# Performance work log

Measured on AMD Instinct MI355X. Metric: run time of the kernel, lower is better.

## Reference

```python
import jax, jax.numpy as jnp
from jax import lax
import numpy as np

BATCH, DIM, HID, NSTEPS = 32768, 128, 256, 50

def setup_inputs() -> dict:
    key = jax.random.key(0)
    k1, k2, k3 = jax.random.split(key, 3)
    inputs = jax.random.normal(k1, (BATCH, DIM), dtype=jnp.float32)
    # increasing timestamps over [0, 1] -> 50 Euler steps of dt = 0.02
    timestamps = jnp.linspace(0.0, 1.0, NSTEPS + 1, dtype=jnp.float32)
    # small init keeps the Euler trajectory stable
    W1 = jax.random.normal(k2, (DIM, HID), dtype=jnp.float32) * 0.05
    b1 = jnp.zeros((HID,), dtype=jnp.float32)
    W2 = jax.random.normal(k3, (HID, DIM), dtype=jnp.float32) * 0.05
    b2 = jnp.zeros((DIM,), dtype=jnp.float32)
    return {"inputs": inputs, "timestamps": timestamps, "W1": W1, "b1": b1, "W2": W2, "b2": b2}

def reference(inputs, timestamps, W1, b1, W2, b2):
    """Euler integration of dh/dt = f(h) = tanh(h@W1+b1)@W2+b2; returns final state h(T).
    Matches AdjointODEFunc.forward (which returns states[-1])."""
    dts = timestamps[1:] - timestamps[:-1]  # [NSTEPS]

    def f(h):  # vector field (time-invariant MLP)
        return jnp.tanh(h @ W1 + b1) @ W2 + b2

    def step(h, dt):
        return h + dt * f(h), None

    h_final, _ = lax.scan(step, inputs, dts)
    return h_final
```

## Files before the change

### kernel.cpp

```cpp
#include <hip/hip_runtime.h>


typedef __attribute__((ext_vector_type(8))) short short8;
typedef __attribute__((ext_vector_type(4))) float float4v;
typedef __attribute__((ext_vector_type(4))) int int4v;

union FB { int4v i; short8 s; };

#define W1F_OFF 0
#define W2F_OFF 65536
#define B1_OFF  131072
#define DT_OFF  132096
#define LDS_BYTES 132352

#define TSCALE 2.8853900817779268f

__device__ __forceinline__ unsigned rne2(float x) {
  unsigned u = __float_as_uint(x);
  return u + 0x7fffu + ((u >> 16) & 1u);
}

#if __has_builtin(__builtin_amdgcn_cvt_pk_bf16_f32)
__device__ __forceinline__ int pk2(float lo, float hi) {
  return __builtin_bit_cast(int, __builtin_amdgcn_cvt_pk_bf16_f32(lo, hi));
}
#else
__device__ __forceinline__ int pk2(float lo, float hi) {
  return (int)__builtin_amdgcn_perm(rne2(hi), rne2(lo), 0x07060302u);
}
#endif

__device__ __forceinline__ int4v packfrag(float4v e, float4v o) {
  int4v f;
  f.x = pk2(e.x, e.y);
  f.y = pk2(e.z, e.w);
  f.z = pk2(o.x, o.y);
  f.w = pk2(o.z, o.w);
  return f;
}

#define MFMA16(a, b, c) __builtin_amdgcn_mfma_f32_16x16x32_bf16(a, b, c, 0, 0, 0)

extern "C" __global__ __launch_bounds__(512)
void ode_kernel(const float* __restrict__ inp, const float* __restrict__ ts,
                const float* __restrict__ W1, const float* __restrict__ b1,
                const float* __restrict__ W2, const float* __restrict__ b2,
                float* __restrict__ out) {
  __shared__ __align__(16) char ldsb[LDS_BYTES];
  float* b1f = (float*)(ldsb + B1_OFF);
  float* dtf = (float*)(ldsb + DT_OFF);

  const int tid = threadIdx.x;
  const int lane = tid & 63, wave = tid >> 6;
  const int ln = lane & 15;
  const int q = lane >> 4;
  const int row = blockIdx.x * 128 + wave * 16 + ln;

  #pragma unroll 1
  for (int it = 0; it < 8; it++) {
    const int pi = it * 512 + tid;
    const int fid = pi >> 6, L = pi & 63;
    const int nt = fid >> 2, c = fid & 3;
    const int lf = L & 15, qf = L >> 4;
    const int n = nt * 16 + lf;
    const int kb = c * 32 + qf * 4;
    float v0 = W1[(kb + 0) * 256 + n] * TSCALE;
    float v1 = W1[(kb + 1) * 256 + n] * TSCALE;
    float v2 = W1[(kb + 2) * 256 + n] * TSCALE;
    float v3 = W1[(kb + 3) * 256 + n] * TSCALE;
    float v4 = W1[(kb + 16) * 256 + n] * TSCALE;
    float v5 = W1[(kb + 17) * 256 + n] * TSCALE;
    float v6 = W1[(kb + 18) * 256 + n] * TSCALE;
    float v7 = W1[(kb + 19) * 256 + n] * TSCALE;
    int4v d = {pk2(v0, v1), pk2(v2, v3), pk2(v4, v5), pk2(v6, v7)};
    *(int4v*)(ldsb + W1F_OFF + pi * 16) = d;
  }
  #pragma unroll 1
  for (int it = 0; it < 8; it++) {
    const int pi = it * 512 + tid;
    const int fid = pi >> 6, L = pi & 63;
    const int p = fid >> 3, tb = fid & 7;
    const int lf = L & 15, qf = L >> 4;
    const int d_out = tb * 16 + lf;
    const int kb = p * 32 + qf * 4;
    float v0 = W2[(kb + 0) * 128 + d_out];
    float v1 = W2[(kb + 1) * 128 + d_out];
    float v2 = W2[(kb + 2) * 128 + d_out];
    float v3 = W2[(kb + 3) * 128 + d_out];
    float v4 = W2[(kb + 16) * 128 + d_out];
    float v5 = W2[(kb + 17) * 128 + d_out];
    float v6 = W2[(kb + 18) * 128 + d_out];
    float v7 = W2[(kb + 19) * 128 + d_out];
    int4v d = {pk2(v0, v1), pk2(v2, v3), pk2(v4, v5), pk2(v6, v7)};
    *(int4v*)(ldsb + W2F_OFF + pi * 16) = d;
  }
  if (tid < 256) b1f[tid] = b1[tid] * TSCALE;
  if (tid < 50) dtf[tid] = ts[tid + 1] - ts[tid];

  float4v b2v[8];
  #pragma unroll
  for (int tb = 0; tb < 8; tb++)
    b2v[tb] = *(const float4v*)&b2[tb * 16 + q * 4];

  float4v h4[8];
  #pragma unroll
  for (int tb = 0; tb < 8; tb++)
    h4[tb] = *(const float4v*)&inp[row * 128 + tb * 16 + q * 4];

  __syncthreads();

  const int4v* w1f = (const int4v*)(ldsb + W1F_OFF) + lane;
  const int4v* w2f = (const int4v*)(ldsb + W2F_OFF) + lane;

  #pragma unroll 1
  for (int s = 0; s < 50; s++) {
    const float dt = dtf[s];
    const float m2dt = -2.0f * dt;

    FB hb[4];
    #pragma unroll
    for (int kc = 0; kc < 4; kc++)
      hb[kc].i = packfrag(h4[2 * kc], h4[2 * kc + 1]);

    #pragma unroll 1
    for (int p = 0; p < 8; p++) {
      const int nt0 = 2 * p, nt1 = 2 * p + 1;
      FB wA[4], wB[4];
      #pragma unroll
      for (int c = 0; c < 4; c++) {
        wA[c].i = w1f[(nt0 * 4 + c) * 64];
        wB[c].i = w1f[(nt1 * 4 + c) * 64];
      }
      float4v g0 = *(const float4v*)&b1f[nt0 * 16 + q * 4];
      float4v g1 = *(const float4v*)&b1f[nt1 * 16 + q * 4];
      #pragma unroll
      for (int c = 0; c < 4; c++) {
        g0 = MFMA16(wA[c].s, hb[c].s, g0);
        g1 = MFMA16(wB[c].s, hb[c].s, g1);
      }

      FB w2r[8];
      #pragma unroll
      for (int tb = 0; tb < 8; tb++)
        w2r[tb].i = w2f[(p * 8 + tb) * 64];

      float4v a0, a1;
      #pragma unroll
      for (int r = 0; r < 4; r++) {
        a0[r] = fmaf(__builtin_amdgcn_rcpf(__builtin_amdgcn_exp2f(g0[r]) + 1.0f), m2dt, dt);
        a1[r] = fmaf(__builtin_amdgcn_rcpf(__builtin_amdgcn_exp2f(g1[r]) + 1.0f), m2dt, dt);
      }
      FB af;
      af.i = packfrag(a0, a1);

      #pragma unroll
      for (int tb = 0; tb < 8; tb++)
        h4[tb] = MFMA16(w2r[tb].s, af.s, h4[tb]);
    }

    #pragma unroll
    for (int tb = 0; tb < 8; tb++)
      #pragma unroll
      for (int r = 0; r < 4; r++)
        h4[tb][r] = fmaf(dt, b2v[tb][r], h4[tb][r]);
  }

  #pragma unroll
  for (int tb = 0; tb < 8; tb++)
    *(float4v*)&out[row * 128 + tb * 16 + q * 4] = h4[tb];
}

extern "C" void kernel_launch(void* const* d_in, const int* in_sizes, int n_in,
                              void* d_out, int out_size, void* d_ws, size_t ws_size,
                              hipStream_t stream) {
  const float* inp = (const float*)d_in[0];
  const float* ts  = (const float*)d_in[1];
  const float* W1  = (const float*)d_in[2];
  const float* b1  = (const float*)d_in[3];
  const float* W2  = (const float*)d_in[4];
  const float* b2  = (const float*)d_in[5];
  hipLaunchKernelGGL(ode_kernel, dim3(256), dim3(512), 0, stream,
                     inp, ts, W1, b1, W2, b2, (float*)d_out);
}
```

Before: 316.6 us.

## Switch MLP matmuls from bf16 to fp8 MFMA with scaled weights

Weights, hidden state, and activations are now quantized to fp8 (with a ×16 scale on weights and activations) and use the 16x16x32 fp8 MFMA instead of bf16. This halves LDS footprint and fragment register size. It also moves b1 into registers and accumulates the second matmul into a separate fp32 accumulator before the dt-scaled update. The aim is to cut MFMA and LDS traffic per step, at a significant accuracy risk: fp8 quantization of the state h compounds over 50 Euler steps.

```diff
diff --git a/kernel.cpp b/kernel.cpp
--- a/kernel.cpp
+++ b/kernel.cpp
@@ -1,45 +1,33 @@
 #include <hip/hip_runtime.h>
 
 
-typedef __attribute__((ext_vector_type(8))) short short8;
 typedef __attribute__((ext_vector_type(4))) float float4v;
-typedef __attribute__((ext_vector_type(4))) int int4v;
+typedef __attribute__((ext_vector_type(2))) int int2v;
 
-union FB { int4v i; short8 s; };
+union F8 { long l; int2v i; };
 
 #define W1F_OFF 0
-#define W2F_OFF 65536
-#define B1_OFF  131072
-#define DT_OFF  132096
-#define LDS_BYTES 132352
+#define W2F_OFF 32768
+#define DT_OFF  65536
+#define LDS_BYTES 65792
 
 #define TSCALE 2.8853900817779268f
+#define WSC 16.0f
 
-__device__ __forceinline__ unsigned rne2(float x) {
-  unsigned u = __float_as_uint(x);
-  return u + 0x7fffu + ((u >> 16) & 1u);
+__device__ __forceinline__ int pk4_fp8(float a, float b, float c, float d) {
+  int v = __builtin_amdgcn_cvt_pk_fp8_f32(a, b, 0, false);
+  v = __builtin_amdgcn_cvt_pk_fp8_f32(c, d, v, true);
+  return v;
 }
 
-#if __has_builtin(__builtin_amdgcn_cvt_pk_bf16_f32)
-__device__ __forceinline__ int pk2(float lo, float hi) {
-  return __builtin_bit_cast(int, __builtin_amdgcn_cvt_pk_bf16_f32(lo, hi));
-}
-#else
-__device__ __forceinline__ int pk2(float lo, float hi) {
-  return (int)__builtin_amdgcn_perm(rne2(hi), rne2(lo), 0x07060302u);
-}
-#endif
-
-__device__ __forceinline__ int4v packfrag(float4v e, float4v o) {
-  int4v f;
-  f.x = pk2(e.x, e.y);
-  f.y = pk2(e.z, e.w);
-  f.z = pk2(o.x, o.y);
-  f.w = pk2(o.z, o.w);
-  return f;
+__device__ __forceinline__ long packfrag8(float4v e, float4v o) {
+  F8 f;
+  f.i.x = pk4_fp8(e.x, e.y, e.z, e.w);
+  f.i.y = pk4_fp8(o.x, o.y, o.z, o.w);
+  return f.l;
 }
 
-#define MFMA16(a, b, c) __builtin_amdgcn_mfma_f32_16x16x32_bf16(a, b, c, 0, 0, 0)
+#define MFMA8(a, b, c) __builtin_amdgcn_mfma_f32_16x16x32_fp8_fp8(a, b, c, 0, 0, 0)
 
 extern "C" __global__ __launch_bounds__(512)
 void ode_kernel(const float* __restrict__ inp, const float* __restrict__ ts,
@@ -47,7 +35,6 @@
                 const float* __restrict__ W2, const float* __restrict__ b2,
                 float* __restrict__ out) {
   __shared__ __align__(16) char ldsb[LDS_BYTES];
-  float* b1f = (float*)(ldsb + B1_OFF);
   float* dtf = (float*)(ldsb + DT_OFF);
 
   const int tid = threadIdx.x;
@@ -64,16 +51,12 @@
     const int lf = L & 15, qf = L >> 4;
     const int n = nt * 16 + lf;
     const int kb = c * 32 + qf * 4;
-    float v0 = W1[(kb + 0) * 256 + n] * TSCALE;
-    float v1 = W1[(kb + 1) * 256 + n] * TSCALE;
-    float v2 = W1[(kb + 2) * 256 + n] * TSCALE;
-    float v3 = W1[(kb + 3) * 256 + n] * TSCALE;
-    float v4 = W1[(kb + 16) * 256 + n] * TSCALE;
-    float v5 = W1[(kb + 17) * 256 + n] * TSCALE;
-    float v6 = W1[(kb + 18) * 256 + n] * TSCALE;
-    float v7 = W1[(kb + 19) * 256 + n] * TSCALE;
-    int4v d = {pk2(v0, v1), pk2(v2, v3), pk2(v4, v5), pk2(v6, v7)};
-    *(int4v*)(ldsb + W1F_OFF + pi * 16) = d;
+    const float sc = WSC * TSCALE;
+    float4v e = {W1[(kb + 0) * 256 + n] * sc, W1[(kb + 1) * 256 + n] * sc,
+                 W1[(kb + 2) * 256 + n] * sc, W1[(kb + 3) * 256 + n] * sc};
+    float4v o = {W1[(kb + 16) * 256 + n] * sc, W1[(kb + 17) * 256 + n] * sc,
+                 W1[(kb + 18) * 256 + n] * sc, W1[(kb + 19) * 256 + n] * sc};
+    *(long*)(ldsb + W1F_OFF + pi * 8) = packfrag8(e, o);
   }
   #pragma unroll 1
   for (int it = 0; it < 8; it++) {
@@ -81,23 +64,22 @@
     const int fid = pi >> 6, L = pi & 63;
     const int p = fid >> 3, tb = fid & 7;
     const int lf = L & 15, qf = L >> 4;
-    const int d_out = tb * 16 + lf;
+    const int dd = tb * 16 + lf;
     const int kb = p * 32 + qf * 4;
-    float v0 = W2[(kb + 0) * 128 + d_out];
-    float v1 = W2[(kb + 1) * 128 + d_out];
-    float v2 = W2[(kb + 2) * 128 + d_out];
-    float v3 = W2[(kb + 3) * 128 + d_out];
-    float v4 = W2[(kb + 16) * 128 + d_out];
-    float v5 = W2[(kb + 17) * 128 + d_out];
-    float v6 = W2[(kb + 18) * 128 + d_out];
-    float v7 = W2[(kb + 19) * 128 + d_out];
-    int4v d = {pk2(v0, v1), pk2(v2, v3), pk2(v4, v5), pk2(v6, v7)};
-    *(int4v*)(ldsb + W2F_OFF + pi * 16) = d;
+    float4v e = {W2[(kb + 0) * 128 + dd] * WSC, W2[(kb + 1) * 128 + dd] * WSC,
+                 W2[(kb + 2) * 128 + dd] * WSC, W2[(kb + 3) * 128 + dd] * WSC};
+    float4v o = {W2[(kb + 16) * 128 + dd] * WSC, W2[(kb + 17) * 128 + dd] * WSC,
+                 W2[(kb + 18) * 128 + dd] * WSC, W2[(kb + 19) * 128 + dd] * WSC};
+    *(long*)(ldsb + W2F_OFF + pi * 8) = packfrag8(e, o);
   }
-  if (tid < 256) b1f[tid] = b1[tid] * TSCALE;
   if (tid < 50) dtf[tid] = ts[tid + 1] - ts[tid];
 
-  float4v b2v[8];
+  float4v b1v[16], b2v[8];
+  #pragma unroll
+  for (int nt = 0; nt < 16; nt++) {
+    float4v v = *(const float4v*)&b1[nt * 16 + q * 4];
+    b1v[nt] = v * (WSC * TSCALE);
+  }
   #pragma unroll
   for (int tb = 0; tb < 8; tb++)
     b2v[tb] = *(const float4v*)&b2[tb * 16 + q * 4];
@@ -109,60 +91,64 @@
 
   __syncthreads();
 
-  const int4v* w1f = (const int4v*)(ldsb + W1F_OFF) + lane;
-  const int4v* w2f = (const int4v*)(ldsb + W2F_OFF) + lane;
+  const long* w1f = (const long*)(ldsb + W1F_OFF) + lane;
+  const long* w2f = (const long*)(ldsb + W2F_OFF) + lane;
 
   #pragma unroll 1
   for (int s = 0; s < 50; s++) {
     const float dt = dtf[s];
-    const float m2dt = -2.0f * dt;
+    const float dts = dt * (1.0f / 256.0f);
 
-    FB hb[4];
+    long hb[4];
     #pragma unroll
     for (int kc = 0; kc < 4; kc++)
-      hb[kc].i = packfrag(h4[2 * kc], h4[2 * kc + 1]);
+      hb[kc] = packfrag8(h4[2 * kc], h4[2 * kc + 1]);
+
+    float4v acc[8];
+    #pragma unroll
+    for (int tb = 0; tb < 8; tb++) acc[tb] = (float4v){0.f, 0.f, 0.f, 0.f};
 
     #pragma unroll 1
     for (int p = 0; p < 8; p++) {
       const int nt0 = 2 * p, nt1 = 2 * p + 1;
-      FB wA[4], wB[4];
+      long wA[4], wB[4];
       #pragma unroll
       for (int c = 0; c < 4; c++) {
-        wA[c].i = w1f[(nt0 * 4 + c) * 64];
-        wB[c].i = w1f[(nt1 * 4 + c) * 64];
+        wA[c] = w1f[(nt0 * 4 + c) * 64];
+        wB[c] = w1f[(nt1 * 4 + c) * 64];
       }
-      float4v g0 = *(const float4v*)&b1f[nt0 * 16 + q * 4];
-      float4v g1 = *(const float4v*)&b1f[nt1 * 16 + q * 4];
+      float4v g0 = b1v[nt0], g1 = b1v[nt1];
       #pragma unroll
       for (int c = 0; c < 4; c++) {
-        g0 = MFMA16(wA[c].s, hb[c].s, g0);
-        g1 = MFMA16(wB[c].s, hb[c].s, g1);
+        g0 = MFMA8(wA[c], hb[c], g0);
+        g1 = MFMA8(wB[c], hb[c], g1);
       }
 
-      FB w2r[8];
+      long w2r[8];
       #pragma unroll
       for (int tb = 0; tb < 8; tb++)
-        w2r[tb].i = w2f[(p * 8 + tb) * 64];
+        w2r[tb] = w2f[(p * 8 + tb) * 64];
 
       float4v a0, a1;
       #pragma unroll
       for (int r = 0; r < 4; r++) {
-        a0[r] = fmaf(__builtin_amdgcn_rcpf(__builtin_amdgcn_exp2f(g0[r]) + 1.0f), m2dt, dt);
-        a1[r] = fmaf(__builtin_amdgcn_rcpf(__builtin_amdgcn_exp2f(g1[r]) + 1.0f), m2dt, dt);
+        a0[r] = fmaf(__builtin_amdgcn_rcpf(
+                    __builtin_amdgcn_exp2f(g0[r] * 0.0625f) + 1.0f), -32.f, 16.f);
+        a1[r] = fmaf(__builtin_amdgcn_rcpf(
+                    __builtin_amdgcn_exp2f(g1[r] * 0.0625f) + 1.0f), -32.f, 16.f);
       }
-      FB af;
-      af.i = packfrag(a0, a1);
+      long af = packfrag8(a0, a1);
 
       #pragma unroll
       for (int tb = 0; tb < 8; tb++)
-        h4[tb] = MFMA16(w2r[tb].s, af.s, h4[tb]);
+        acc[tb] = MFMA8(w2r[tb], af, acc[tb]);
     }
 
     #pragma unroll
     for (int tb = 0; tb < 8; tb++)
       #pragma unroll
       for (int r = 0; r < 4; r++)
-        h4[tb][r] = fmaf(dt, b2v[tb][r], h4[tb][r]);
+        h4[tb][r] = fmaf(dts, acc[tb][r], fmaf(dt, b2v[tb][r], h4[tb][r]));
   }
 
   #pragma unroll
```

Measured after the change: 355.3 us. 1.12x slower.
